# Kernel optimization log

Measured on AMD Instinct MI355X. Metric: run time of the kernel, lower is better.

Reference implementation:

```python
import jax, jax.numpy as jnp
import numpy as np

N_POINTS = 8192
N_TOPICS = 64
B = 524288


def setup_inputs() -> dict:
    key = jax.random.key(0)
    k1, k2, k3, k4 = jax.random.split(key, 4)
    pij = jax.random.uniform(k1, (B,), dtype=jnp.float32, minval=1e-6, maxval=1.0)
    i = jax.random.randint(k2, (B,), 0, N_POINTS, dtype=jnp.int64)
    j = jax.random.randint(k3, (B,), 0, N_POINTS, dtype=jnp.int64)
    W = jax.random.normal(k4, (N_POINTS, N_TOPICS), dtype=jnp.float32)  # nn.Embedding weight
    return {"pij": pij, "i": i, "j": j, "W": W}


def reference(pij, i, j, W):
    # pairwise squared distances over ALL points, via the gram trick
    # (avoids materializing the [n, n, d] broadcasted tensor of the torch code)
    sq = jnp.sum(W * W, axis=1)                       # [n]
    d2 = sq[:, None] + sq[None, :] - 2.0 * (W @ W.T)  # [n, n]
    d2 = jnp.maximum(d2, 0.0)                         # numerical floor (exact math is >= 0)
    n = W.shape[0]
    # Cauchy kernel partition: sum_{k,l} 1/(1+d2) minus the n diagonal ones
    part = jnp.sum(1.0 / (1.0 + d2)) - jnp.asarray(n, d2.dtype)
    xi = W[i]                                         # [B, d]
    xj = W[j]                                         # [B, d]
    # FAITHFUL to source: (1 + diff^2).sum(1) adds 1 per dim => n_topics + ||xi-xj||^2
    num = 1.0 / jnp.sum(1.0 + (xi - xj) ** 2, axis=1)  # [B]
    qij = num / part
    loss_kld = pij * (jnp.log(pij) - jnp.log(qij))
    return jnp.sum(loss_kld)
```

## Files before the change

kernel.cpp:

```cpp
#include <hip/hip_runtime.h>
#include <math.h>

#define NPOINTS   8192
#define NDIM      64
#define TILE      128
#define NT2       64
#define NBLK      2080
#define NGRP      512

#define WS_W16   0
#define WS_W8    262144
#define WS_SQ    393216
#define WS_PARTA 401408
#define WS_A1P   403488
#define WS_A3P   407584

typedef __attribute__((ext_vector_type(8))) short bf16x8;
typedef __attribute__((ext_vector_type(4))) float f32x4;
typedef __attribute__((ext_vector_type(2))) float f32x2;

__device__ inline unsigned f2bf_pk(float lo, float hi) {
    unsigned ul = __float_as_uint(lo), uh = __float_as_uint(hi);
    ul += 0x7FFFu + ((ul >> 16) & 1u);
    uh += 0x7FFFu + ((uh >> 16) & 1u);
    return (ul >> 16) | (uh & 0xFFFF0000u);
}
template <bool HI>
__device__ inline f32x2 cvt2(unsigned dw) {
    return __builtin_amdgcn_cvt_pk_f32_fp8((int)dw, HI);
}
__device__ inline void sqacc(f32x2& s, unsigned a, unsigned b) {
    f32x2 dl = cvt2<false>(a) - cvt2<false>(b);
    f32x2 dh = cvt2<true >(a) - cvt2<true >(b);
    s += dl * dl;
    s += dh * dh;
}
__device__ inline float d2_16(const uint4 x[4], const uint4 y[4]) {
    f32x2 s2 = {0.f, 0.f};
    #pragma unroll
    for (int k = 0; k < 4; ++k) {
        sqacc(s2, x[k].x, y[k].x); sqacc(s2, x[k].y, y[k].y);
        sqacc(s2, x[k].z, y[k].z); sqacc(s2, x[k].w, y[k].w);
    }
    return s2.x + s2.y;
}

__global__ __launch_bounds__(256) void prep_kernel(const float* __restrict__ W,
                                                   float* __restrict__ sq,
                                                   unsigned* __restrict__ W16f,
                                                   unsigned* __restrict__ W8) {
    int g = blockIdx.x;
    int t = threadIdx.x;

    {
        int h = t >> 7, L = (t >> 1) & 63, dp = t & 1;
        int row = g * 16 + (L & 15), quad = L >> 4;
        float4 v = *(const float4*)(W + row * NDIM + h * 32 + quad * 8 + dp * 4);
        uint2 o;
        o.x = f2bf_pk(v.x, v.y);
        o.y = f2bf_pk(v.z, v.w);
        *(uint2*)(W16f + ((g * 2 + h) * 256 + L * 4 + dp * 2)) = o;
    }
    {
        int r = t >> 4, s = t & 15;
        float4 v = *(const float4*)(W + (g * 16 + r) * NDIM + s * 4);
        float p = v.x * v.x + v.y * v.y + v.z * v.z + v.w * v.w;
        p += __shfl_xor(p, 1, 64);
        p += __shfl_xor(p, 2, 64);
        p += __shfl_xor(p, 4, 64);
        p += __shfl_xor(p, 8, 64);
        if (s == 0) sq[g * 16 + r] = p;
    }
    {
        int r = g * 16 + (t >> 4), d = t & 15;
        float4 x = *(const float4*)(W + r * NDIM + d * 4);
        int lo = __builtin_amdgcn_cvt_pk_fp8_f32(x.x, x.y, 0, false);
        int dw = __builtin_amdgcn_cvt_pk_fp8_f32(x.z, x.w, lo, true);
        W8[r * 16 + d] = (unsigned)dw;
    }
}

__global__ __launch_bounds__(256) void fused_kernel(
        const unsigned* __restrict__ W16f, const float* __restrict__ sq,
        float* __restrict__ partA,
        const unsigned* __restrict__ W8, const float* __restrict__ pij,
        const int* __restrict__ ii, const int* __restrict__ jj, int nb,
        float* __restrict__ a1p, float* __restrict__ a3p, int npb2) {
    int t = threadIdx.x;
    int z = blockIdx.x;
    __shared__ float red[8];
    __shared__ float wsum[4];

    int twop = npb2 * 2;
    bool isPair;
    int job;
    if (z < twop) { isPair = (z & 1) != 0; job = z >> 1; }
    else          { isPair = false;        job = npb2 + (z - twop); }

    if (isPair) {
        int p1 = job * 512 + t;
        int p2 = p1 + 256;
        bool v1 = p1 < nb, v2 = p2 < nb;
        int i1 = 0, j1 = 0, i2 = 0, j2 = 0;
        float q1 = 0.f, q2 = 0.f;
        if (v1) { i1 = ii[p1]; j1 = jj[p1]; q1 = pij[p1]; }
        if (v2) { i2 = ii[p2]; j2 = jj[p2]; q2 = pij[p2]; }
        const uint4* X1 = (const uint4*)(W8 + i1 * 16);
        const uint4* Y1 = (const uint4*)(W8 + j1 * 16);
        const uint4* X2 = (const uint4*)(W8 + i2 * 16);
        const uint4* Y2 = (const uint4*)(W8 + j2 * 16);
        uint4 xa[4], ya[4], xb[4], yb[4];
        #pragma unroll
        for (int k = 0; k < 4; ++k) xa[k] = X1[k];
        #pragma unroll
        for (int k = 0; k < 4; ++k) ya[k] = Y1[k];
        #pragma unroll
        for (int k = 0; k < 4; ++k) xb[k] = X2[k];
        #pragma unroll
        for (int k = 0; k < 4; ++k) yb[k] = Y2[k];
        float a1 = 0.f, a3 = 0.f;
        float da = d2_16(xa, ya);
        float db = d2_16(xb, yb);
        if (v1) { a1  = q1 * __logf(q1 * ((float)NDIM + da)); a3  = q1; }
        if (v2) { a1 += q2 * __logf(q2 * ((float)NDIM + db)); a3 += q2; }
        #pragma unroll
        for (int m = 32; m >= 1; m >>= 1) {
            a1 += __shfl_xor(a1, m, 64);
            a3 += __shfl_xor(a3, m, 64);
        }
        if ((t & 63) == 0) { red[t >> 6] = a1; red[4 + (t >> 6)] = a3; }
        __syncthreads();
        if (t == 0) {
            a1p[job] = red[0] + red[1] + red[2] + red[3];
            a3p[job] = red[4] + red[5] + red[6] + red[7];
        }
    } else {
        int zt = job;
        int w = t >> 6, lane = t & 63;
        int by = (int)((129.0f - sqrtf((float)(16641 - 8 * zt))) * 0.5f);
        while (by * NT2 - by * (by - 1) / 2 > zt) --by;
        while ((by + 1) * NT2 - (by + 1) * by / 2 <= zt) ++by;
        int bx = by + (zt - (by * NT2 - by * (by - 1) / 2));

        int wm = w >> 1, wn = w & 1, quad = lane >> 4, l15 = lane & 15;
        int a0 = by * TILE, b0 = bx * TILE;

        f32x4 acc[4][4];
        #pragma unroll
        for (int i = 0; i < 4; ++i)
            #pragma unroll
            for (int j = 0; j < 4; ++j) acc[i][j] = (f32x4){0.f, 0.f, 0.f, 0.f};

        int gA = (a0 >> 4) + wm * 4;
        int gB = (b0 >> 4) + wn * 4;
        #pragma unroll
        for (int h = 0; h < 2; ++h) {
            bf16x8 af[4], bfr[4];
            #pragma unroll
            for (int tm = 0; tm < 4; ++tm)
                af[tm] = *(const bf16x8*)(W16f + (((gA + tm) * 2 + h) * 256 + lane * 4));
            #pragma unroll
            for (int tn = 0; tn < 4; ++tn)
                bfr[tn] = *(const bf16x8*)(W16f + (((gB + tn) * 2 + h) * 256 + lane * 4));
            #pragma unroll
            for (int tm = 0; tm < 4; ++tm)
                #pragma unroll
                for (int tn = 0; tn < 4; ++tn)
                    acc[tm][tn] = __builtin_amdgcn_mfma_f32_16x16x32_bf16(af[tm], bfr[tn],
                                                                          acc[tm][tn], 0, 0, 0);
        }

        float4 base1[4];
        float  sqb[4];
        {
            int arow = a0 + wm * 64 + quad * 4;
            #pragma unroll
            for (int tm = 0; tm < 4; ++tm) {
                float4 v = *(const float4*)(sq + arow + tm * 16);
                base1[tm] = (float4){1.0f + v.x, 1.0f + v.y, 1.0f + v.z, 1.0f + v.w};
            }
            int bcol = b0 + wn * 64 + l15;
            #pragma unroll
            for (int tn = 0; tn < 4; ++tn) sqb[tn] = sq[bcol + tn * 16];
        }

        float ssum = 0.f;
        if (bx > by) {
            #pragma unroll
            for (int tn = 0; tn < 4; ++tn) {
                float c0 = sqb[tn];
                #pragma unroll
                for (int tm = 0; tm < 4; ++tm) {
                    ssum += __builtin_amdgcn_rcpf(fmaf(acc[tm][tn][0], -2.0f, base1[tm].x + c0));
                    ssum += __builtin_amdgcn_rcpf(fmaf(acc[tm][tn][1], -2.0f, base1[tm].y + c0));
                    ssum += __builtin_amdgcn_rcpf(fmaf(acc[tm][tn][2], -2.0f, base1[tm].z + c0));
                    ssum += __builtin_amdgcn_rcpf(fmaf(acc[tm][tn][3], -2.0f, base1[tm].w + c0));
                }
            }
        } else {
            int quad4 = quad * 4;
            #pragma unroll
            for (int tn = 0; tn < 4; ++tn) {
                int cl = wn * 64 + tn * 16 + l15;
                float c0 = sqb[tn];
                float b4[4];
                #pragma unroll
                for (int tm = 0; tm < 4; ++tm) {
                    b4[0] = base1[tm].x; b4[1] = base1[tm].y;
                    b4[2] = base1[tm].z; b4[3] = base1[tm].w;
                    #pragma unroll
                    for (int r = 0; r < 4; ++r) {
                        int rl = wm * 64 + tm * 16 + quad4 + r;
                        float inv = __builtin_amdgcn_rcpf(fmaf(acc[tm][tn][r], -2.0f, b4[r] + c0));
                        ssum += (cl > rl) ? inv : 0.f;
                    }
                }
            }
        }
        #pragma unroll
        for (int m = 32; m >= 1; m >>= 1) ssum += __shfl_xor(ssum, m, 64);
        if (lane == 0) wsum[w] = ssum;
        __syncthreads();
        if (t == 0) partA[zt] = wsum[0] + wsum[1] + wsum[2] + wsum[3];
    }
}

__global__ __launch_bounds__(256) void final_kernel(const float* __restrict__ partA,
                                                    const float* __restrict__ a1p,
                                                    const float* __restrict__ a3p,
                                                    int npb,
                                                    float* __restrict__ out) {
    __shared__ double r1[256], r2[256], r3[256];
    int t = threadIdx.x;
    double dpart = 0.0, d1 = 0.0, d3 = 0.0;
    for (int k = t; k < NBLK; k += 256) dpart += (double)partA[k];
    for (int k = t; k < npb; k += 256) { d1 += (double)a1p[k]; d3 += (double)a3p[k]; }
    r1[t] = dpart; r2[t] = d1; r3[t] = d3;
    __syncthreads();
    for (int s = 128; s >= 1; s >>= 1) {
        if (t < s) { r1[t] += r1[t + s]; r2[t] += r2[t + s]; r3[t] += r3[t + s]; }
        __syncthreads();
    }
    if (t == 0) {
        double part = 2.0 * r1[0];
        out[0] = (float)(r2[0] + r3[0] * log(part));
    }
}

extern "C" void kernel_launch(void* const* d_in, const int* in_sizes, int n_in,
                              void* d_out, int out_size, void* d_ws, size_t ws_size,
                              hipStream_t stream) {
    const float* pij = (const float*)d_in[0];
    const int*   ii  = (const int*)d_in[1];
    const int*   jj  = (const int*)d_in[2];
    const float* W   = (const float*)d_in[3];
    float* out = (float*)d_out;
    float* ws  = (float*)d_ws;

    unsigned* W16f  = (unsigned*)ws + WS_W16;
    unsigned* W8    = (unsigned*)ws + WS_W8;
    float*    sqv   = ws + WS_SQ;
    float*    partA = ws + WS_PARTA;
    float*    a1p   = ws + WS_A1P;
    float*    a3p   = ws + WS_A3P;

    int nb   = in_sizes[0];
    int npb2 = (nb + 511) / 512;

    prep_kernel<<<NGRP, 256, 0, stream>>>(W, sqv, W16f, W8);
    fused_kernel<<<NBLK + npb2, 256, 0, stream>>>(W16f, sqv, partA,
                                                  W8, pij, ii, jj, nb,
                                                  a1p, a3p, npb2);
    final_kernel<<<1, 256, 0, stream>>>(partA, a1p, a3p, npb2, out);
}
```

Before: 96.36 us.

## Split fused kernel into separate pair and pairwise-distance kernels

Result: slower. 99.07 us (+2.8%).

```diff
diff --git a/kernel.cpp b/kernel.cpp
--- a/kernel.cpp
+++ b/kernel.cpp
@@ -80,149 +80,145 @@
     }
 }
 
-__global__ __launch_bounds__(256) void fused_kernel(
-        const unsigned* __restrict__ W16f, const float* __restrict__ sq,
-        float* __restrict__ partA,
-        const unsigned* __restrict__ W8, const float* __restrict__ pij,
-        const int* __restrict__ ii, const int* __restrict__ jj, int nb,
-        float* __restrict__ a1p, float* __restrict__ a3p, int npb2) {
+__global__ __launch_bounds__(256) void pair_kernel(const unsigned* __restrict__ W8,
+                                                   const float* __restrict__ pij,
+                                                   const int* __restrict__ ii,
+                                                   const int* __restrict__ jj,
+                                                   int nb,
+                                                   float* __restrict__ a1p,
+                                                   float* __restrict__ a3p) {
     int t = threadIdx.x;
+    int job = blockIdx.x;
+    int p1 = job * 512 + t;
+    int p2 = p1 + 256;
+    bool v1 = p1 < nb, v2 = p2 < nb;
+    int i1 = 0, j1 = 0, i2 = 0, j2 = 0;
+    float q1 = 0.f, q2 = 0.f;
+    if (v1) { i1 = ii[p1]; j1 = jj[p1]; q1 = pij[p1]; }
+    if (v2) { i2 = ii[p2]; j2 = jj[p2]; q2 = pij[p2]; }
+    const uint4* X1 = (const uint4*)(W8 + i1 * 16);
+    const uint4* Y1 = (const uint4*)(W8 + j1 * 16);
+    const uint4* X2 = (const uint4*)(W8 + i2 * 16);
+    const uint4* Y2 = (const uint4*)(W8 + j2 * 16);
+    uint4 xa[4], ya[4], xb[4], yb[4];
+    #pragma unroll
+    for (int k = 0; k < 4; ++k) xa[k] = X1[k];
+    #pragma unroll
+    for (int k = 0; k < 4; ++k) ya[k] = Y1[k];
+    #pragma unroll
+    for (int k = 0; k < 4; ++k) xb[k] = X2[k];
+    #pragma unroll
+    for (int k = 0; k < 4; ++k) yb[k] = Y2[k];
+    float da = d2_16(xa, ya);
+    float db = d2_16(xb, yb);
+    float a1 = 0.f, a3 = 0.f;
+    if (v1) { a1  = q1 * __logf(q1 * ((float)NDIM + da)); a3  = q1; }
+    if (v2) { a1 += q2 * __logf(q2 * ((float)NDIM + db)); a3 += q2; }
+    #pragma unroll
+    for (int m = 32; m >= 1; m >>= 1) {
+        a1 += __shfl_xor(a1, m, 64);
+        a3 += __shfl_xor(a3, m, 64);
+    }
+    __shared__ float red[8];
+    if ((t & 63) == 0) { red[t >> 6] = a1; red[4 + (t >> 6)] = a3; }
+    __syncthreads();
+    if (t == 0) {
+        a1p[job] = red[0] + red[1] + red[2] + red[3];
+        a3p[job] = red[4] + red[5] + red[6] + red[7];
+    }
+}
+
+__global__ __launch_bounds__(256) void pairwise_kernel(const unsigned* __restrict__ W16f,
+                                                       const float* __restrict__ sq,
+                                                       float* __restrict__ partA) {
     int z = blockIdx.x;
-    __shared__ float red[8];
-    __shared__ float wsum[4];
-
-    int twop = npb2 * 2;
-    bool isPair;
-    int job;
-    if (z < twop) { isPair = (z & 1) != 0; job = z >> 1; }
-    else          { isPair = false;        job = npb2 + (z - twop); }
-
-    if (isPair) {
-        int p1 = job * 512 + t;
-        int p2 = p1 + 256;
-        bool v1 = p1 < nb, v2 = p2 < nb;
-        int i1 = 0, j1 = 0, i2 = 0, j2 = 0;
-        float q1 = 0.f, q2 = 0.f;
-        if (v1) { i1 = ii[p1]; j1 = jj[p1]; q1 = pij[p1]; }
-        if (v2) { i2 = ii[p2]; j2 = jj[p2]; q2 = pij[p2]; }
-        const uint4* X1 = (const uint4*)(W8 + i1 * 16);
-        const uint4* Y1 = (const uint4*)(W8 + j1 * 16);
-        const uint4* X2 = (const uint4*)(W8 + i2 * 16);
-        const uint4* Y2 = (const uint4*)(W8 + j2 * 16);
-        uint4 xa[4], ya[4], xb[4], yb[4];
-        #pragma unroll
-        for (int k = 0; k < 4; ++k) xa[k] = X1[k];
-        #pragma unroll
-        for (int k = 0; k < 4; ++k) ya[k] = Y1[k];
-        #pragma unroll
-        for (int k = 0; k < 4; ++k) xb[k] = X2[k];
-        #pragma unroll
-        for (int k = 0; k < 4; ++k) yb[k] = Y2[k];
-        float a1 = 0.f, a3 = 0.f;
-        float da = d2_16(xa, ya);
-        float db = d2_16(xb, yb);
-        if (v1) { a1  = q1 * __logf(q1 * ((float)NDIM + da)); a3  = q1; }
-        if (v2) { a1 += q2 * __logf(q2 * ((float)NDIM + db)); a3 += q2; }
-        #pragma unroll
-        for (int m = 32; m >= 1; m >>= 1) {
-            a1 += __shfl_xor(a1, m, 64);
-            a3 += __shfl_xor(a3, m, 64);
+    int t = threadIdx.x, w = t >> 6, lane = t & 63;
+    int by = (int)((129.0f - sqrtf((float)(16641 - 8 * z))) * 0.5f);
+    while (by * NT2 - by * (by - 1) / 2 > z) --by;
+    while ((by + 1) * NT2 - (by + 1) * by / 2 <= z) ++by;
+    int bx = by + (z - (by * NT2 - by * (by - 1) / 2));
+
+    int wm = w >> 1, wn = w & 1, quad = lane >> 4, l15 = lane & 15;
+    int a0 = by * TILE, b0 = bx * TILE;
+
+    float4 base1[4];
+    float  sqb[4];
+    {
+        int arow = a0 + wm * 64 + quad * 4;
+        #pragma unroll
+        for (int tm = 0; tm < 4; ++tm) {
+            float4 v = *(const float4*)(sq + arow + tm * 16);
+            base1[tm] = (float4){1.0f + v.x, 1.0f + v.y, 1.0f + v.z, 1.0f + v.w};
         }
-        if ((t & 63) == 0) { red[t >> 6] = a1; red[4 + (t >> 6)] = a3; }
-        __syncthreads();
-        if (t == 0) {
-            a1p[job] = red[0] + red[1] + red[2] + red[3];
-            a3p[job] = red[4] + red[5] + red[6] + red[7];
+        int bcol = b0 + wn * 64 + l15;
+        #pragma unroll
+        for (int tn = 0; tn < 4; ++tn) sqb[tn] = sq[bcol + tn * 16];
+    }
+
+    f32x4 acc[4][4];
+    #pragma unroll
+    for (int i = 0; i < 4; ++i)
+        #pragma unroll
+        for (int j = 0; j < 4; ++j) acc[i][j] = (f32x4){0.f, 0.f, 0.f, 0.f};
+
+    int gA = (a0 >> 4) + wm * 4;
+    int gB = (b0 >> 4) + wn * 4;
+    #pragma unroll
+    for (int h = 0; h < 2; ++h) {
+        bf16x8 af[4], bfr[4];
+        #pragma unroll
+        for (int tm = 0; tm < 4; ++tm)
+            af[tm] = *(const bf16x8*)(W16f + (((gA + tm) * 2 + h) * 256 + lane * 4));
+        #pragma unroll
+        for (int tn = 0; tn < 4; ++tn)
+            bfr[tn] = *(const bf16x8*)(W16f + (((gB + tn) * 2 + h) * 256 + lane * 4));
+        #pragma unroll
+        for (int tm = 0; tm < 4; ++tm)
+            #pragma unroll
+            for (int tn = 0; tn < 4; ++tn)
+                acc[tm][tn] = __builtin_amdgcn_mfma_f32_16x16x32_bf16(af[tm], bfr[tn],
+                                                                      acc[tm][tn], 0, 0, 0);
+    }
+
+    float ssum = 0.f;
+    if (bx > by) {
+        #pragma unroll
+        for (int tn = 0; tn < 4; ++tn) {
+            float c0 = sqb[tn];
+            #pragma unroll
+            for (int tm = 0; tm < 4; ++tm) {
+                ssum += __builtin_amdgcn_rcpf(fmaf(acc[tm][tn][0], -2.0f, base1[tm].x + c0));
+                ssum += __builtin_amdgcn_rcpf(fmaf(acc[tm][tn][1], -2.0f, base1[tm].y + c0));
+                ssum += __builtin_amdgcn_rcpf(fmaf(acc[tm][tn][2], -2.0f, base1[tm].z + c0));
+                ssum += __builtin_amdgcn_rcpf(fmaf(acc[tm][tn][3], -2.0f, base1[tm].w + c0));
+            }
         }
     } else {
-        int zt = job;
-        int w = t >> 6, lane = t & 63;
-        int by = (int)((129.0f - sqrtf((float)(16641 - 8 * zt))) * 0.5f);
-        while (by * NT2 - by * (by - 1) / 2 > zt) --by;
-        while ((by + 1) * NT2 - (by + 1) * by / 2 <= zt) ++by;
-        int bx = by + (zt - (by * NT2 - by * (by - 1) / 2));
-
-        int wm = w >> 1, wn = w & 1, quad = lane >> 4, l15 = lane & 15;
-        int a0 = by * TILE, b0 = bx * TILE;
-
-        f32x4 acc[4][4];
-        #pragma unroll
-        for (int i = 0; i < 4; ++i)
-            #pragma unroll
-            for (int j = 0; j < 4; ++j) acc[i][j] = (f32x4){0.f, 0.f, 0.f, 0.f};
-
-        int gA = (a0 >> 4) + wm * 4;
-        int gB = (b0 >> 4) + wn * 4;
-        #pragma unroll
-        for (int h = 0; h < 2; ++h) {
-            bf16x8 af[4], bfr[4];
-            #pragma unroll
-            for (int tm = 0; tm < 4; ++tm)
-                af[tm] = *(const bf16x8*)(W16f + (((gA + tm) * 2 + h) * 256 + lane * 4));
-            #pragma unroll
-            for (int tn = 0; tn < 4; ++tn)
-                bfr[tn] = *(const bf16x8*)(W16f + (((gB + tn) * 2 + h) * 256 + lane * 4));
-            #pragma unroll
-            for (int tm = 0; tm < 4; ++tm)
-                #pragma unroll
-                for (int tn = 0; tn < 4; ++tn)
-                    acc[tm][tn] = __builtin_amdgcn_mfma_f32_16x16x32_bf16(af[tm], bfr[tn],
-                                                                          acc[tm][tn], 0, 0, 0);
-        }
-
-        float4 base1[4];
-        float  sqb[4];
-        {
-            int arow = a0 + wm * 64 + quad * 4;
+        int quad4 = quad * 4;
+        #pragma unroll
+        for (int tn = 0; tn < 4; ++tn) {
+            int cl = wn * 64 + tn * 16 + l15;
+            float c0 = sqb[tn];
+            float b4[4];
             #pragma unroll
             for (int tm = 0; tm < 4; ++tm) {
-                float4 v = *(const float4*)(sq + arow + tm * 16);
-                base1[tm] = (float4){1.0f + v.x, 1.0f + v.y, 1.0f + v.z, 1.0f + v.w};
-            }
-            int bcol = b0 + wn * 64 + l15;
-            #pragma unroll
-            for (int tn = 0; tn < 4; ++tn) sqb[tn] = sq[bcol + tn * 16];
-        }
-
-        float ssum = 0.f;
-        if (bx > by) {
-            #pragma unroll
-            for (int tn = 0; tn < 4; ++tn) {
-                float c0 = sqb[tn];
+                b4[0] = base1[tm].x; b4[1] = base1[tm].y;
+                b4[2] = base1[tm].z; b4[3] = base1[tm].w;
                 #pragma unroll
-                for (int tm = 0; tm < 4; ++tm) {
-                    ssum += __builtin_amdgcn_rcpf(fmaf(acc[tm][tn][0], -2.0f, base1[tm].x + c0));
-                    ssum += __builtin_amdgcn_rcpf(fmaf(acc[tm][tn][1], -2.0f, base1[tm].y + c0));
-                    ssum += __builtin_amdgcn_rcpf(fmaf(acc[tm][tn][2], -2.0f, base1[tm].z + c0));
-                    ssum += __builtin_amdgcn_rcpf(fmaf(acc[tm][tn][3], -2.0f, base1[tm].w + c0));
-                }
-            }
-        } else {
-            int quad4 = quad * 4;
-            #pragma unroll
-            for (int tn = 0; tn < 4; ++tn) {
-                int cl = wn * 64 + tn * 16 + l15;
-                float c0 = sqb[tn];
-                float b4[4];
-                #pragma unroll
-                for (int tm = 0; tm < 4; ++tm) {
-                    b4[0] = base1[tm].x; b4[1] = base1[tm].y;
-                    b4[2] = base1[tm].z; b4[3] = base1[tm].w;
-                    #pragma unroll
-                    for (int r = 0; r < 4; ++r) {
-                        int rl = wm * 64 + tm * 16 + quad4 + r;
-                        float inv = __builtin_amdgcn_rcpf(fmaf(acc[tm][tn][r], -2.0f, b4[r] + c0));
-                        ssum += (cl > rl) ? inv : 0.f;
-                    }
+                for (int r = 0; r < 4; ++r) {
+                    int rl = wm * 64 + tm * 16 + quad4 + r;
+                    float inv = __builtin_amdgcn_rcpf(fmaf(acc[tm][tn][r], -2.0f, b4[r] + c0));
+                    ssum += (cl > rl) ? inv : 0.f;
                 }
             }
         }
-        #pragma unroll
-        for (int m = 32; m >= 1; m >>= 1) ssum += __shfl_xor(ssum, m, 64);
-        if (lane == 0) wsum[w] = ssum;
-        __syncthreads();
-        if (t == 0) partA[zt] = wsum[0] + wsum[1] + wsum[2] + wsum[3];
-    }
+    }
+    #pragma unroll
+    for (int m = 32; m >= 1; m >>= 1) ssum += __shfl_xor(ssum, m, 64);
+    __shared__ float wsum[4];
+    if (lane == 0) wsum[w] = ssum;
+    __syncthreads();
+    if (t == 0) partA[z] = wsum[0] + wsum[1] + wsum[2] + wsum[3];
 }
 
 __global__ __launch_bounds__(256) void final_kernel(const float* __restrict__ partA,
@@ -268,8 +264,7 @@
     int npb2 = (nb + 511) / 512;
 
     prep_kernel<<<NGRP, 256, 0, stream>>>(W, sqv, W16f, W8);
-    fused_kernel<<<NBLK + npb2, 256, 0, stream>>>(W16f, sqv, partA,
-                                                  W8, pij, ii, jj, nb,
-                                                  a1p, a3p, npb2);
+    pair_kernel<<<npb2, 256, 0, stream>>>(W8, pij, ii, jj, nb, a1p, a3p);
+    pairwise_kernel<<<NBLK, 256, 0, stream>>>(W16f, sqv, partA);
     final_kernel<<<1, 256, 0, stream>>>(partA, a1p, a3p, npb2, out);
 }
```
